# Optimization experiments

Hardware: AMD Instinct MI355X
Metric: run time of the kernel (lower is better)

## Reference

```python
import jax, jax.numpy as jnp
import numpy as np

EPS = 1e-5  # equinox LayerNorm default eps

def setup_inputs() -> dict:
    key = jax.random.key(0)
    k1, k2, k3, k4, k5 = jax.random.split(key, 5)
    heads, d, dH, N = 16, 1024, 64, 2048
    # lecun-normal-ish scaling for fan_in=d
    s = 1.0 / np.sqrt(d)
    return {
        "x": jax.random.normal(k1, (d, N), dtype=jnp.float32),
        "WQ": jax.random.normal(k2, (heads, d, dH), dtype=jnp.float32) * s,
        "WK": jax.random.normal(k3, (heads, d, dH), dtype=jnp.float32) * s,
        "WV": jax.random.normal(k4, (heads, d, dH), dtype=jnp.float32) * s,
        "W0": jax.random.normal(k5, (d, d), dtype=jnp.float32) * s,
    }

def reference(x, WQ, WK, WV, W0):
    # x: [d, N]
    residual = x
    # equinox LayerNorm over full shape (d, N), no affine params
    mean = jnp.mean(x)
    var = jnp.var(x)
    xn = (x - mean) * jax.lax.rsqrt(var + EPS)
    # project: [h, d_model, dH] x [d_model, N] -> [h, dH, N]
    Q = jnp.einsum('hcd,ci->hdi', WQ, xn)
    K = jnp.einsum('hcd,ci->hdi', WK, xn)
    V = jnp.einsum('hcd,ci->hdi', WV, xn)
    dH = WK.shape[-1]
    dot = jnp.einsum('hdi,hdj->hij', Q, K)  # [h, N, N]
    alpha = jax.nn.softmax(dot / jnp.sqrt(jnp.asarray(dH, dot.dtype)), axis=-1)
    attn = jnp.einsum('hij,hdj->hdi', alpha, V)  # [h, dH, N]
    N = attn.shape[2]
    attn = attn.reshape(-1, N)  # [d, N]
    out = W0 @ attn
    return out + residual
```

## Files before the change

kernel.cpp:

```cpp
#include <hip/hip_runtime.h>
#include <math.h>

typedef unsigned short u16;
typedef _Float16 f16;
typedef __attribute__((ext_vector_type(8))) short bf16x8;
typedef __attribute__((ext_vector_type(4))) float f32x4;
typedef __attribute__((ext_vector_type(4))) f16 f16x4;

#define D_MODEL 1024
#define SEQ_N   2048
#define HEADS   16
#define DHEAD   64
#define M3      3072
#define JSPLIT  4
#define JCHUNK  (SEQ_N / JSPLIT)

#define GLOBAL_AS __attribute__((address_space(1)))
#define LDS_AS    __attribute__((address_space(3)))
#define ASYNC16(gp, lp) __builtin_amdgcn_global_load_lds( \
    (const GLOBAL_AS unsigned int*)(gp), (LDS_AS unsigned int*)(lp), 16, 0, 0)

__device__ __forceinline__ u16 f2bf(float f) {
  union { float f; unsigned int u; } v; v.f = f;
  unsigned int r = v.u + 0x7fffu + ((v.u >> 16) & 1u);
  return (u16)(r >> 16);
}

__global__ __launch_bounds__(256) void ln_reduce1(const float* __restrict__ x,
                                                  double* __restrict__ part, int n4) {
  const float4* x4 = (const float4*)x;
  double s = 0.0, ss = 0.0;
  for (int idx = blockIdx.x * blockDim.x + threadIdx.x; idx < n4;
       idx += gridDim.x * blockDim.x) {
    float4 v = x4[idx];
    s  += (double)v.x + (double)v.y + (double)v.z + (double)v.w;
    ss += (double)v.x * v.x + (double)v.y * v.y + (double)v.z * v.z + (double)v.w * v.w;
  }
  __shared__ double ls[256], lss[256];
  int t = threadIdx.x;
  ls[t] = s; lss[t] = ss;
  __syncthreads();
  for (int off = 128; off > 0; off >>= 1) {
    if (t < off) { ls[t] += ls[t + off]; lss[t] += lss[t + off]; }
    __syncthreads();
  }
  if (t == 0) { part[2 * blockIdx.x] = ls[0]; part[2 * blockIdx.x + 1] = lss[0]; }
}

__global__ __launch_bounds__(256) void ln_reduce2(const double* __restrict__ part,
                                                  float* __restrict__ stats) {
  __shared__ double ls[256], lss[256];
  int t = threadIdx.x;
  ls[t] = part[2 * t]; lss[t] = part[2 * t + 1];
  __syncthreads();
  for (int off = 128; off > 0; off >>= 1) {
    if (t < off) { ls[t] += ls[t + off]; lss[t] += lss[t + off]; }
    __syncthreads();
  }
  if (t == 0) {
    double inv = 1.0 / ((double)D_MODEL * (double)SEQ_N);
    double mean = ls[0] * inv;
    double var  = lss[0] * inv - mean * mean;
    stats[0] = (float)mean;
    stats[1] = (float)(1.0 / sqrt(var + 1e-5));
  }
}

__global__ __launch_bounds__(256) void ln_norm_t(const float* __restrict__ x,
                                                 const float* __restrict__ stats,
                                                 u16* __restrict__ xnt) {
  __shared__ float tile[64][65];
  float mean = stats[0], rstd = stats[1];
  int t = threadIdx.x;
  int ib = blockIdx.x * 64, cb = blockIdx.y * 64;
  int il = t & 63, cl = t >> 6;
  for (int r = 0; r < 16; ++r) {
    int c = cl + r * 4;
    tile[c][il] = (x[(size_t)(cb + c) * SEQ_N + ib + il] - mean) * rstd;
  }
  __syncthreads();
  int c2 = t & 63, i2 = t >> 6;
  for (int r = 0; r < 16; ++r) {
    int i = i2 + r * 4;
    xnt[(size_t)(ib + i) * D_MODEL + cb + c2] = f2bf(tile[c2][i]);
  }
}

__global__ __launch_bounds__(256) void pack_qkv(const float* __restrict__ WQ,
                                                const float* __restrict__ WK,
                                                const float* __restrict__ WV,
                                                u16* __restrict__ Wp) {
  __shared__ float tile[32][65];
  const float* W = (blockIdx.z == 0) ? WQ : ((blockIdx.z == 1) ? WK : WV);
  int h = blockIdx.y, cb = blockIdx.x * 32;
  int t = threadIdx.x;
  int dh = t & 63, cl = t >> 6;
  for (int r = 0; r < 8; ++r) {
    int c = cl + r * 4;
    tile[c][dh] = W[((size_t)h * D_MODEL + cb + c) * DHEAD + dh];
  }
  __syncthreads();
  int c2 = t & 31, d2 = t >> 5;
  for (int r = 0; r < 8; ++r) {
    int dd = d2 + r * 8;
    Wp[(size_t)((blockIdx.z * HEADS + h) * DHEAD + dd) * D_MODEL + cb + c2] =
        f2bf(tile[c2][dd]);
  }
}

__global__ __launch_bounds__(256) void pack_w0(const float* __restrict__ W0,
                                               u16* __restrict__ W0p, int n4) {
  int idx = blockIdx.x * blockDim.x + threadIdx.x;
  if (idx >= n4) return;
  float4 v = ((const float4*)W0)[idx];
  unsigned int lo = (unsigned int)f2bf(v.x) | ((unsigned int)f2bf(v.y) << 16);
  unsigned int hi = (unsigned int)f2bf(v.z) | ((unsigned int)f2bf(v.w) << 16);
  uint2 o; o.x = lo; o.y = hi;
  *(uint2*)(&W0p[(size_t)idx * 4]) = o;
}

__global__ __launch_bounds__(256) void gemm_qkv(const u16* __restrict__ A,
                                                const u16* __restrict__ Bt,
                                                u16* __restrict__ Qt,
                                                u16* __restrict__ Kt,
                                                f16* __restrict__ Vb) {
  __shared__ __align__(16) u16 Alds[128 * 32];
  __shared__ __align__(16) u16 Blds[64 * 32];
  int t = threadIdx.x;
  int lane = t & 63, w = t >> 6;
  int g = lane >> 4, l16 = lane & 15;
  int mb = blockIdx.y * 128, nb = blockIdx.x * 64;

  f32x4 acc[2][4];
#pragma unroll
  for (int i = 0; i < 2; ++i)
#pragma unroll
    for (int j = 0; j < 4; ++j) acc[i][j] = (f32x4){0.f, 0.f, 0.f, 0.f};

  int srow = t >> 2, scol = (t & 3) * 8;
  const u16* Ag0 = A + (size_t)(mb + srow) * D_MODEL + scol;
  const u16* Ag1 = A + (size_t)(mb + 64 + srow) * D_MODEL + scol;
  const u16* Bg  = Bt + (size_t)(nb + srow) * D_MODEL + scol;

  for (int kb = 0; kb < D_MODEL; kb += 32) {
    ASYNC16(Ag0 + kb, &Alds[t * 8]);
    ASYNC16(Ag1 + kb, &Alds[2048 + t * 8]);
    ASYNC16(Bg + kb, &Blds[t * 8]);
    __syncthreads();
    bf16x8 af[2], bf[4];
#pragma unroll
    for (int tm = 0; tm < 2; ++tm)
      af[tm] = *(const bf16x8*)(&Alds[(w * 32 + tm * 16 + l16) * 32 + g * 8]);
#pragma unroll
    for (int tn = 0; tn < 4; ++tn)
      bf[tn] = *(const bf16x8*)(&Blds[(tn * 16 + l16) * 32 + g * 8]);
#pragma unroll
    for (int tm = 0; tm < 2; ++tm)
#pragma unroll
      for (int tn = 0; tn < 4; ++tn)
        acc[tm][tn] = __builtin_amdgcn_mfma_f32_16x16x32_bf16(af[tm], bf[tn],
                                                              acc[tm][tn], 0, 0, 0);
    __syncthreads();
  }

#pragma unroll
  for (int tm = 0; tm < 2; ++tm) {
    int row0 = mb + w * 32 + tm * 16 + g * 4;
#pragma unroll
    for (int tn = 0; tn < 4; ++tn) {
      int col = nb + tn * 16 + l16;
      if (mb < 2 * D_MODEL) {
        u16* T = (mb < D_MODEL) ? Qt : Kt;
        int rbase = (mb < D_MODEL) ? row0 : row0 - D_MODEL;
        ushort4 o;
        o.x = f2bf(acc[tm][tn][0]); o.y = f2bf(acc[tm][tn][1]);
        o.z = f2bf(acc[tm][tn][2]); o.w = f2bf(acc[tm][tn][3]);
        *(ushort4*)(&T[(size_t)col * D_MODEL + rbase]) = o;
      } else {
        int rbase = row0 - 2 * D_MODEL;
#pragma unroll
        for (int r = 0; r < 4; ++r)
          Vb[(size_t)(rbase + r) * SEQ_N + col] = (f16)acc[tm][tn][r];
      }
    }
  }
}

__global__ __launch_bounds__(256) void gemm_bf16(const u16* __restrict__ A,
                                                 const u16* __restrict__ Bt,
                                                 float* __restrict__ C,
                                                 const float* __restrict__ res,
                                                 int M, int N, int K) {
  __shared__ __align__(16) u16 Alds[64 * 32];
  __shared__ __align__(16) u16 Blds[64 * 32];
  int t = threadIdx.x;
  int w = t >> 6, lane = t & 63;
  int g = lane >> 4, l16 = lane & 15;
  int mb = blockIdx.y * 64, nb = blockIdx.x * 64;
  f32x4 acc[4];
  for (int i = 0; i < 4; ++i) acc[i] = (f32x4){0.f, 0.f, 0.f, 0.f};
  int srow = t >> 2, scol = (t & 3) * 8;
  const u16* Ag = A + (size_t)(mb + srow) * K + scol;
  const u16* Bg = Bt + (size_t)(nb + srow) * K + scol;
  for (int kb = 0; kb < K; kb += 32) {
    ASYNC16(Ag + kb, &Alds[t * 8]);
    ASYNC16(Bg + kb, &Blds[t * 8]);
    __syncthreads();
    bf16x8 af = *(const bf16x8*)(&Alds[(w * 16 + l16) * 32 + g * 8]);
#pragma unroll
    for (int tn = 0; tn < 4; ++tn) {
      bf16x8 bf = *(const bf16x8*)(&Blds[(tn * 16 + l16) * 32 + g * 8]);
      acc[tn] = __builtin_amdgcn_mfma_f32_16x16x32_bf16(af, bf, acc[tn], 0, 0, 0);
    }
    __syncthreads();
  }
  int col0 = nb + l16;
  int row0 = mb + w * 16 + g * 4;
#pragma unroll
  for (int tn = 0; tn < 4; ++tn) {
    int col = col0 + tn * 16;
#pragma unroll
    for (int r = 0; r < 4; ++r) {
      int row = row0 + r;
      float v = acc[tn][r];
      if (res) v += res[(size_t)row * N + col];
      C[(size_t)row * N + col] = v;
    }
  }
}

__global__ __launch_bounds__(256, 8) void attn_mfma(const u16* __restrict__ Qt,
                                                    const u16* __restrict__ Kt,
                                                    const f16* __restrict__ Vb,
                                                    f16* __restrict__ Opart,
                                                    float* __restrict__ Lpart) {
  __shared__ __align__(16) u16 Klds[64][72];
  __shared__ __align__(16) f16 Vlds[64][72];
  int h = blockIdx.y;
  int ib = blockIdx.x * 64;
  int sp = blockIdx.z;
  int j0 = sp * JCHUNK;
  int t = threadIdx.x;
  int w = t >> 6, lane = t & 63;
  int g = lane >> 4, l16 = lane & 15;

  bf16x8 bq[2];
  {
    const u16* qb = Qt + (size_t)(ib + w * 16 + l16) * D_MODEL + h * DHEAD + g * 8;
    bq[0] = *(const bf16x8*)(qb);
    bq[1] = *(const bf16x8*)(qb + 32);
  }

  f32x4 acc_o[4];
#pragma unroll
  for (int i = 0; i < 4; ++i) acc_o[i] = (f32x4){0.f, 0.f, 0.f, 0.f};
  float lsum = 0.f;

  int srow = t >> 3, sch = (t & 7) * 8;
  for (int it = 0; it < JCHUNK / 64; ++it) {
    int jb = j0 + it * 64;
    uint4 kr0 = *(const uint4*)(&Kt[(size_t)(jb + srow) * D_MODEL + h * DHEAD + sch]);
    uint4 kr1 = *(const uint4*)(&Kt[(size_t)(jb + srow + 32) * D_MODEL + h * DHEAD + sch]);
    uint4 vr0 = *(const uint4*)(&Vb[(size_t)(h * DHEAD + srow) * SEQ_N + jb + sch]);
    uint4 vr1 = *(const uint4*)(&Vb[(size_t)(h * DHEAD + srow + 32) * SEQ_N + jb + sch]);
    *(uint4*)(&Klds[srow][sch]) = kr0;
    *(uint4*)(&Klds[srow + 32][sch]) = kr1;
    *(uint4*)(&Vlds[srow][sch]) = vr0;
    *(uint4*)(&Vlds[srow + 32][sch]) = vr1;
    __syncthreads();

    f32x4 s[4];
#pragma unroll
    for (int i = 0; i < 4; ++i) s[i] = (f32x4){0.f, 0.f, 0.f, 0.f};
#pragma unroll
    for (int kk = 0; kk < 2; ++kk)
#pragma unroll
      for (int tn = 0; tn < 4; ++tn) {
        bf16x8 ak = *(const bf16x8*)(&Klds[tn * 16 + l16][kk * 32 + g * 8]);
        s[tn] = __builtin_amdgcn_mfma_f32_16x16x32_bf16(ak, bq[kk], s[tn], 0, 0, 0);
      }
    f16x4 pf[4];
#pragma unroll
    for (int tn = 0; tn < 4; ++tn)
#pragma unroll
      for (int r = 0; r < 4; ++r) {
        float pv = __expf(fmaf(s[tn][r], 0.125f, -4.0f));
        lsum += pv;
        pf[tn][r] = (f16)pv;
      }
#pragma unroll
    for (int tn = 0; tn < 4; ++tn)
#pragma unroll
      for (int td = 0; td < 4; ++td) {
        f16x4 bv = *(const f16x4*)(&Vlds[td * 16 + l16][tn * 16 + g * 4]);
        acc_o[td] =
            __builtin_amdgcn_mfma_f32_16x16x16f16(pf[tn], bv, acc_o[td], 0, 0, 0);
      }
    __syncthreads();
  }

  lsum += __shfl_xor(lsum, 16, 64);
  lsum += __shfl_xor(lsum, 32, 64);
  if (g == 0)
    Lpart[((size_t)sp * HEADS + h) * SEQ_N + ib + w * 16 + l16] = lsum;

#pragma unroll
  for (int td = 0; td < 4; ++td) {
    int dh = h * DHEAD + td * 16 + l16;
#pragma unroll
    for (int r = 0; r < 4; ++r) {
      int i = ib + w * 16 + g * 4 + r;
      Opart[((size_t)sp * SEQ_N + i) * D_MODEL + dh] = (f16)acc_o[td][r];
    }
  }
}

__global__ __launch_bounds__(256) void attn_combine(const f16* __restrict__ Opart,
                                                    const float* __restrict__ Lpart,
                                                    u16* __restrict__ attnt) {
  int i = blockIdx.x;
  int c = threadIdx.x * 4;
  int h = c >> 6;
  float l = 0.f;
#pragma unroll
  for (int s = 0; s < JSPLIT; ++s) l += Lpart[((size_t)s * HEADS + h) * SEQ_N + i];
  float o[4] = {0.f, 0.f, 0.f, 0.f};
#pragma unroll
  for (int s = 0; s < JSPLIT; ++s) {
    f16x4 v = *(const f16x4*)(&Opart[((size_t)s * SEQ_N + i) * D_MODEL + c]);
#pragma unroll
    for (int r = 0; r < 4; ++r) o[r] += (float)v[r];
  }
  float inv = 1.0f / l;
  ushort4 ob;
  ob.x = f2bf(o[0] * inv); ob.y = f2bf(o[1] * inv);
  ob.z = f2bf(o[2] * inv); ob.w = f2bf(o[3] * inv);
  *(ushort4*)(&attnt[(size_t)i * D_MODEL + c]) = ob;
}

extern "C" void kernel_launch(void* const* d_in, const int* in_sizes, int n_in,
                              void* d_out, int out_size, void* d_ws, size_t ws_size,
                              hipStream_t stream) {
  const float* x  = (const float*)d_in[0];
  const float* WQ = (const float*)d_in[1];
  const float* WK = (const float*)d_in[2];
  const float* WV = (const float*)d_in[3];
  const float* W0 = (const float*)d_in[4];
  float* out = (float*)d_out;

  char* ws = (char*)d_ws;
  size_t off = 0;
  double* part  = (double*)(ws + off); off += 8192;
  float*  stats = (float*)(part + 512);
  u16*    xnt   = (u16*)(ws + off); off += (size_t)SEQ_N * D_MODEL * 2;
  u16*    Wp    = (u16*)(ws + off); off += (size_t)M3 * D_MODEL * 2;
  u16*    W0p   = (u16*)(ws + off); off += (size_t)D_MODEL * D_MODEL * 2;
  u16*    Qt    = (u16*)(ws + off); off += (size_t)SEQ_N * D_MODEL * 2;
  u16*    Kt    = (u16*)(ws + off); off += (size_t)SEQ_N * D_MODEL * 2;
  f16*    Vb    = (f16*)(ws + off); off += (size_t)D_MODEL * SEQ_N * 2;
  u16*    attnt = (u16*)(ws + off); off += (size_t)SEQ_N * D_MODEL * 2;
  f16*    Opart = (f16*)(ws + off); off += (size_t)JSPLIT * SEQ_N * D_MODEL * 2;
  float*  Lpart = (float*)(ws + off); off += (size_t)JSPLIT * HEADS * SEQ_N * 4;

  ln_reduce1<<<256, 256, 0, stream>>>(x, part, (D_MODEL * SEQ_N) / 4);
  ln_reduce2<<<1, 256, 0, stream>>>(part, stats);
  ln_norm_t<<<dim3(SEQ_N / 64, D_MODEL / 64), 256, 0, stream>>>(x, stats, xnt);
  pack_qkv<<<dim3(D_MODEL / 32, HEADS, 3), 256, 0, stream>>>(WQ, WK, WV, Wp);
  pack_w0<<<(D_MODEL * D_MODEL / 4 + 255) / 256, 256, 0, stream>>>(W0, W0p,
                                                                   D_MODEL * D_MODEL / 4);
  gemm_qkv<<<dim3(SEQ_N / 64, M3 / 128), 256, 0, stream>>>(Wp, xnt, Qt, Kt, Vb);
  attn_mfma<<<dim3(SEQ_N / 64, HEADS, JSPLIT), 256, 0, stream>>>(Qt, Kt, Vb, Opart, Lpart);
  attn_combine<<<SEQ_N, 256, 0, stream>>>(Opart, Lpart, attnt);
  gemm_bf16<<<dim3(SEQ_N / 64, D_MODEL / 64), 256, 0, stream>>>(W0p, attnt, out, x,
                                                                D_MODEL, SEQ_N, D_MODEL);
}
```

Baseline: 172.8 us.

## Fuse LN stats reduce into normalize, vectorize transpose, halve GEMM barriers, use exp2

Removes the single-block ln_reduce2 launch. Each ln_norm_t block now re-reduces the 512 partial sums redundantly, and the normalize/transpose kernel uses float4 loads and 16-byte bf16 stores. Both GEMMs now load two 32-wide K slices per barrier pair, which halves the synchronisation count at the cost of doubled LDS. The softmax exponent switches from __expf to exp2f with pre-scaled constants. The redundant per-block reduction adds work in the 512 normalize blocks.

After: 183.4 us. 1.06x slower.

```diff
diff --git a/kernel.cpp b/kernel.cpp
--- a/kernel.cpp
+++ b/kernel.cpp
@@ -4,6 +4,7 @@
 typedef unsigned short u16;
 typedef _Float16 f16;
 typedef __attribute__((ext_vector_type(8))) short bf16x8;
+typedef __attribute__((ext_vector_type(8))) unsigned short u16x8;
 typedef __attribute__((ext_vector_type(4))) float f32x4;
 typedef __attribute__((ext_vector_type(4))) f16 f16x4;
 
@@ -47,42 +48,53 @@
   if (t == 0) { part[2 * blockIdx.x] = ls[0]; part[2 * blockIdx.x + 1] = lss[0]; }
 }
 
-__global__ __launch_bounds__(256) void ln_reduce2(const double* __restrict__ part,
-                                                  float* __restrict__ stats) {
-  __shared__ double ls[256], lss[256];
-  int t = threadIdx.x;
-  ls[t] = part[2 * t]; lss[t] = part[2 * t + 1];
-  __syncthreads();
-  for (int off = 128; off > 0; off >>= 1) {
-    if (t < off) { ls[t] += ls[t + off]; lss[t] += lss[t + off]; }
-    __syncthreads();
-  }
-  if (t == 0) {
-    double inv = 1.0 / ((double)D_MODEL * (double)SEQ_N);
-    double mean = ls[0] * inv;
-    double var  = lss[0] * inv - mean * mean;
-    stats[0] = (float)mean;
-    stats[1] = (float)(1.0 / sqrt(var + 1e-5));
-  }
-}
-
 __global__ __launch_bounds__(256) void ln_norm_t(const float* __restrict__ x,
-                                                 const float* __restrict__ stats,
+                                                 const double* __restrict__ part,
                                                  u16* __restrict__ xnt) {
   __shared__ float tile[64][65];
-  float mean = stats[0], rstd = stats[1];
-  int t = threadIdx.x;
+  __shared__ float sstat[2];
+  int t = threadIdx.x;
+  {
+    double* ls = (double*)&tile[0][0];
+    double* lss = ls + 256;
+    ls[t]  = part[2 * t] + part[2 * (t + 256)];
+    lss[t] = part[2 * t + 1] + part[2 * (t + 256) + 1];
+    __syncthreads();
+    for (int off = 128; off > 0; off >>= 1) {
+      if (t < off) { ls[t] += ls[t + off]; lss[t] += lss[t + off]; }
+      __syncthreads();
+    }
+    if (t == 0) {
+      double inv = 1.0 / ((double)D_MODEL * (double)SEQ_N);
+      double mean = ls[0] * inv;
+      double var  = lss[0] * inv - mean * mean;
+      sstat[0] = (float)mean;
+      sstat[1] = (float)(1.0 / sqrt(var + 1e-5));
+    }
+    __syncthreads();
+  }
+  float mean = sstat[0], rstd = sstat[1];
   int ib = blockIdx.x * 64, cb = blockIdx.y * 64;
-  int il = t & 63, cl = t >> 6;
-  for (int r = 0; r < 16; ++r) {
-    int c = cl + r * 4;
-    tile[c][il] = (x[(size_t)(cb + c) * SEQ_N + ib + il] - mean) * rstd;
-  }
   __syncthreads();
-  int c2 = t & 63, i2 = t >> 6;
-  for (int r = 0; r < 16; ++r) {
-    int i = i2 + r * 4;
-    xnt[(size_t)(ib + i) * D_MODEL + cb + c2] = f2bf(tile[c2][i]);
+#pragma unroll
+  for (int r = 0; r < 4; ++r) {
+    int c = (t >> 4) + r * 16;
+    int i4 = (t & 15) * 4;
+    float4 v = *(const float4*)(&x[(size_t)(cb + c) * SEQ_N + ib + i4]);
+    tile[c][i4 + 0] = (v.x - mean) * rstd;
+    tile[c][i4 + 1] = (v.y - mean) * rstd;
+    tile[c][i4 + 2] = (v.z - mean) * rstd;
+    tile[c][i4 + 3] = (v.w - mean) * rstd;
+  }
+  __syncthreads();
+#pragma unroll
+  for (int r = 0; r < 2; ++r) {
+    int i = (t >> 3) + r * 32;
+    int c8 = (t & 7) * 8;
+    u16x8 o;
+#pragma unroll
+    for (int j = 0; j < 8; ++j) o[j] = f2bf(tile[c8 + j][i]);
+    *(u16x8*)(&xnt[(size_t)(ib + i) * D_MODEL + cb + c8]) = o;
   }
 }
 
@@ -124,8 +136,8 @@
                                                 u16* __restrict__ Qt,
                                                 u16* __restrict__ Kt,
                                                 f16* __restrict__ Vb) {
-  __shared__ __align__(16) u16 Alds[128 * 32];
-  __shared__ __align__(16) u16 Blds[64 * 32];
+  __shared__ __align__(16) u16 Alds[2][128 * 32];
+  __shared__ __align__(16) u16 Blds[2][64 * 32];
   int t = threadIdx.x;
   int lane = t & 63, w = t >> 6;
   int g = lane >> 4, l16 = lane & 15;
@@ -142,24 +154,31 @@
   const u16* Ag1 = A + (size_t)(mb + 64 + srow) * D_MODEL + scol;
   const u16* Bg  = Bt + (size_t)(nb + srow) * D_MODEL + scol;
 
-  for (int kb = 0; kb < D_MODEL; kb += 32) {
-    ASYNC16(Ag0 + kb, &Alds[t * 8]);
-    ASYNC16(Ag1 + kb, &Alds[2048 + t * 8]);
-    ASYNC16(Bg + kb, &Blds[t * 8]);
-    __syncthreads();
-    bf16x8 af[2], bf[4];
-#pragma unroll
-    for (int tm = 0; tm < 2; ++tm)
-      af[tm] = *(const bf16x8*)(&Alds[(w * 32 + tm * 16 + l16) * 32 + g * 8]);
-#pragma unroll
-    for (int tn = 0; tn < 4; ++tn)
-      bf[tn] = *(const bf16x8*)(&Blds[(tn * 16 + l16) * 32 + g * 8]);
-#pragma unroll
-    for (int tm = 0; tm < 2; ++tm)
+  for (int kb = 0; kb < D_MODEL; kb += 64) {
+#pragma unroll
+    for (int hh = 0; hh < 2; ++hh) {
+      int ko = kb + hh * 32;
+      ASYNC16(Ag0 + ko, &Alds[hh][t * 8]);
+      ASYNC16(Ag1 + ko, &Alds[hh][2048 + t * 8]);
+      ASYNC16(Bg + ko, &Blds[hh][t * 8]);
+    }
+    __syncthreads();
+#pragma unroll
+    for (int hh = 0; hh < 2; ++hh) {
+      bf16x8 af[2], bf[4];
+#pragma unroll
+      for (int tm = 0; tm < 2; ++tm)
+        af[tm] = *(const bf16x8*)(&Alds[hh][(w * 32 + tm * 16 + l16) * 32 + g * 8]);
 #pragma unroll
       for (int tn = 0; tn < 4; ++tn)
-        acc[tm][tn] = __builtin_amdgcn_mfma_f32_16x16x32_bf16(af[tm], bf[tn],
-                                                              acc[tm][tn], 0, 0, 0);
+        bf[tn] = *(const bf16x8*)(&Blds[hh][(tn * 16 + l16) * 32 + g * 8]);
+#pragma unroll
+      for (int tm = 0; tm < 2; ++tm)
+#pragma unroll
+        for (int tn = 0; tn < 4; ++tn)
+          acc[tm][tn] = __builtin_amdgcn_mfma_f32_16x16x32_bf16(af[tm], bf[tn],
+                                                                acc[tm][tn], 0, 0, 0);
+    }
     __syncthreads();
   }
 
@@ -191,8 +210,8 @@
                                                  float* __restrict__ C,
                                                  const float* __restrict__ res,
                                                  int M, int N, int K) {
-  __shared__ __align__(16) u16 Alds[64 * 32];
-  __shared__ __align__(16) u16 Blds[64 * 32];
+  __shared__ __align__(16) u16 Alds[2][64 * 32];
+  __shared__ __align__(16) u16 Blds[2][64 * 32];
   int t = threadIdx.x;
   int w = t >> 6, lane = t & 63;
   int g = lane >> 4, l16 = lane & 15;
@@ -202,15 +221,22 @@
   int srow = t >> 2, scol = (t & 3) * 8;
   const u16* Ag = A + (size_t)(mb + srow) * K + scol;
   const u16* Bg = Bt + (size_t)(nb + srow) * K + scol;
-  for (int kb = 0; kb < K; kb += 32) {
-    ASYNC16(Ag + kb, &Alds[t * 8]);
-    ASYNC16(Bg + kb, &Blds[t * 8]);
-    __syncthreads();
-    bf16x8 af = *(const bf16x8*)(&Alds[(w * 16 + l16) * 32 + g * 8]);
-#pragma unroll
-    for (int tn = 0; tn < 4; ++tn) {
-      bf16x8 bf = *(const bf16x8*)(&Blds[(tn * 16 + l16) * 32 + g * 8]);
-      acc[tn] = __builtin_amdgcn_mfma_f32_16x16x32_bf16(af, bf, acc[tn], 0, 0, 0);
+  for (int kb = 0; kb < K; kb += 64) {
+#pragma unroll
+    for (int hh = 0; hh < 2; ++hh) {
+      int ko = kb + hh * 32;
+      ASYNC16(Ag + ko, &Alds[hh][t * 8]);
+      ASYNC16(Bg + ko, &Blds[hh][t * 8]);
+    }
+    __syncthreads();
+#pragma unroll
+    for (int hh = 0; hh < 2; ++hh) {
+      bf16x8 af = *(const bf16x8*)(&Alds[hh][(w * 16 + l16) * 32 + g * 8]);
+#pragma unroll
+      for (int tn = 0; tn < 4; ++tn) {
+        bf16x8 bf = *(const bf16x8*)(&Blds[hh][(tn * 16 + l16) * 32 + g * 8]);
+        acc[tn] = __builtin_amdgcn_mfma_f32_16x16x32_bf16(af, bf, acc[tn], 0, 0, 0);
+      }
     }
     __syncthreads();
   }
@@ -284,7 +310,7 @@
     for (int tn = 0; tn < 4; ++tn)
 #pragma unroll
       for (int r = 0; r < 4; ++r) {
-        float pv = __expf(fmaf(s[tn][r], 0.125f, -4.0f));
+        float pv = exp2f(fmaf(s[tn][r], 0.18033688f, -5.7707801f));
         lsum += pv;
         pf[tn][r] = (f16)pv;
       }
@@ -351,7 +377,6 @@
   char* ws = (char*)d_ws;
   size_t off = 0;
   double* part  = (double*)(ws + off); off += 8192;
-  float*  stats = (float*)(part + 512);
   u16*    xnt   = (u16*)(ws + off); off += (size_t)SEQ_N * D_MODEL * 2;
   u16*    Wp    = (u16*)(ws + off); off += (size_t)M3 * D_MODEL * 2;
   u16*    W0p   = (u16*)(ws + off); off += (size_t)D_MODEL * D_MODEL * 2;
@@ -362,9 +387,8 @@
   f16*    Opart = (f16*)(ws + off); off += (size_t)JSPLIT * SEQ_N * D_MODEL * 2;
   float*  Lpart = (float*)(ws + off); off += (size_t)JSPLIT * HEADS * SEQ_N * 4;
 
-  ln_reduce1<<<256, 256, 0, stream>>>(x, part, (D_MODEL * SEQ_N) / 4);
-  ln_reduce2<<<1, 256, 0, stream>>>(part, stats);
-  ln_norm_t<<<dim3(SEQ_N / 64, D_MODEL / 64), 256, 0, stream>>>(x, stats, xnt);
+  ln_reduce1<<<512, 256, 0, stream>>>(x, part, (D_MODEL * SEQ_N) / 4);
+  ln_norm_t<<<dim3(SEQ_N / 64, D_MODEL / 64), 256, 0, stream>>>(x, part, xnt);
   pack_qkv<<<dim3(D_MODEL / 32, HEADS, 3), 256, 0, stream>>>(WQ, WK, WV, Wp);
   pack_w0<<<(D_MODEL * D_MODEL / 4 + 255) / 256, 256, 0, stream>>>(W0, W0p,
                                                                    D_MODEL * D_MODEL / 4);
```
